# Kernel optimization log

Measured on AMD Instinct MI355X. Metric: run time of the kernel, lower is better.

Reference implementation:

```python
import jax, jax.numpy as jnp
import numpy as np

N_NODES = 100000
N_EDGES = 600000
IN_CH = 128
HID = 128


def setup_inputs() -> dict:
    key = jax.random.key(0)
    ks = jax.random.split(key, 8)
    x = jax.random.normal(ks[0], (N_NODES, IN_CH), dtype=jnp.float32)
    edge_index = jax.random.randint(ks[1], (2, N_EDGES), 0, N_NODES, dtype=jnp.int64)
    # Linear weights stored as (in, out); scaled like torch default init
    W1 = jax.random.normal(ks[2], (2 * IN_CH, HID), dtype=jnp.float32) / np.sqrt(2 * IN_CH)
    b1 = jnp.zeros((HID,), dtype=jnp.float32)
    W2 = jax.random.normal(ks[3], (HID, HID), dtype=jnp.float32) / np.sqrt(HID)
    b2 = jnp.zeros((HID,), dtype=jnp.float32)
    W3 = jax.random.normal(ks[4], (HID, 1), dtype=jnp.float32) / np.sqrt(HID)
    b3 = jnp.zeros((1,), dtype=jnp.float32)
    return {"x": x, "edge_index": edge_index, "W1": W1, "b1": b1,
            "W2": W2, "b2": b2, "W3": W3, "b3": b3}


def reference(x, edge_index, W1, b1, W2, b2, W3, b3):
    src = edge_index[0]
    tgt = edge_index[1]
    # gather + concat: [n_edges, 2*in_channels]
    h = jnp.concatenate([x[src, :], x[tgt, :]], axis=1)
    h = jax.nn.elu(h @ W1 + b1)
    h = jax.nn.elu(h @ W2 + b2)
    h = h @ W3 + b3  # [n_edges, 1]
    return jnp.squeeze(h)  # squeeze=True path -> [n_edges]
```

## Files before the change

### kernel.cpp

```cpp
#include <hip/hip_runtime.h>

#define N_NODES 100000
#define N_EDGES 600000
#define NT1 1563
#define NT2 9375
#define LDH 136
#define LDO 264
typedef _Float16 f16x8 __attribute__((ext_vector_type(8)));
typedef _Float16 f16x4 __attribute__((ext_vector_type(4)));
typedef __attribute__((ext_vector_type(4))) float f32x4;

__device__ __forceinline__ float elu_f(float v) {
    return v > 0.0f ? v : (__expf(v) - 1.0f);
}

extern "C" __global__ __launch_bounds__(256, 3)
void k1_node_linear(const float* __restrict__ x, const float* __restrict__ W1,
                    _Float16* __restrict__ P) {
    __shared__ __align__(16) _Float16 sX[64 * LDH];
    __shared__ __align__(16) _Float16 sOut[64 * LDO];

    const int t = threadIdx.x;
    const int w = t >> 6, lane = t & 63;
    const int ln = lane & 15, kg = lane >> 4;

    f16x8 bf[2][2][4];
#pragma unroll
    for (int half = 0; half < 2; ++half)
#pragma unroll
        for (int c = 0; c < 2; ++c) {
            const int n = w * 32 + c * 16 + ln;
#pragma unroll
            for (int ks = 0; ks < 4; ++ks) {
                f16x8 v;
#pragma unroll
                for (int j = 0; j < 8; ++j) {
                    int k = half * 128 + ks * 32 + kg * 8 + j;
                    v[j] = (_Float16)W1[k * 128 + n];
                }
                bf[half][c][ks] = v;
            }
        }

    for (int tile = blockIdx.x; tile < NT1; tile += gridDim.x) {
        const int n0 = tile * 64;

        {
            const size_t fbase = (size_t)n0 * 128;
#pragma unroll
            for (int i = 0; i < 8; ++i) {
                const int f = t * 4 + i * 1024;
                float4 a = make_float4(0.f, 0.f, 0.f, 0.f);
                if (fbase + (size_t)f < (size_t)N_NODES * 128)
                    a = *(const float4*)(x + fbase + f);
                f16x4 h;
                h[0] = (_Float16)a.x; h[1] = (_Float16)a.y;
                h[2] = (_Float16)a.z; h[3] = (_Float16)a.w;
                *(f16x4*)(&sX[(f >> 7) * LDH + (f & 127)]) = h;
            }
        }
        __syncthreads();

        f32x4 acc[2][4][2];
#pragma unroll
        for (int half = 0; half < 2; ++half)
#pragma unroll
            for (int rt = 0; rt < 4; ++rt)
#pragma unroll
                for (int c = 0; c < 2; ++c) acc[half][rt][c] = (f32x4){0.f, 0.f, 0.f, 0.f};

#pragma unroll
        for (int ks = 0; ks < 4; ++ks) {
#pragma unroll
            for (int rt = 0; rt < 4; ++rt) {
                f16x8 a = *(const f16x8*)(&sX[(rt * 16 + ln) * LDH + ks * 32 + kg * 8]);
#pragma unroll
                for (int half = 0; half < 2; ++half)
#pragma unroll
                    for (int c = 0; c < 2; ++c)
                        acc[half][rt][c] = __builtin_amdgcn_mfma_f32_16x16x32_f16(
                            a, bf[half][c][ks], acc[half][rt][c], 0, 0, 0);
            }
        }
        __syncthreads();

#pragma unroll
        for (int half = 0; half < 2; ++half)
#pragma unroll
            for (int rt = 0; rt < 4; ++rt)
#pragma unroll
                for (int c = 0; c < 2; ++c) {
                    const int col = half * 128 + w * 32 + c * 16 + ln;
#pragma unroll
                    for (int reg = 0; reg < 4; ++reg) {
                        const int row = rt * 16 + kg * 4 + reg;
                        sOut[row * LDO + col] = (_Float16)acc[half][rt][c][reg];
                    }
                }
        __syncthreads();

        {
            const size_t ebase = (size_t)n0 * 256;
#pragma unroll
            for (int i = 0; i < 8; ++i) {
                const int e = t * 8 + i * 2048;
                if (n0 + (e >> 8) < N_NODES) {
                    f16x8 v = *(const f16x8*)(&sOut[(e >> 8) * LDO + (e & 255)]);
                    *(f16x8*)(P + ebase + e) = v;
                }
            }
        }
    }
}

extern "C" __global__ __launch_bounds__(256, 3)
void k2_edge_mlp(const _Float16* __restrict__ P, const void* __restrict__ eiv,
                 const float* __restrict__ b1, const float* __restrict__ W2,
                 const float* __restrict__ b2, const float* __restrict__ W3,
                 const float* __restrict__ b3, float* __restrict__ out) {
    __shared__ __align__(16) _Float16 sH[2][64 * LDH];
    __shared__ float sPart[2][4][64];
    __shared__ int sFlag;

    const int t = threadIdx.x;
    const int w = t >> 6, lane = t & 63;
    const int ln = lane & 15, kg = lane >> 4;
    const int row = t >> 2;
    const int kc0 = (t & 3) * 4;
    const float b3v = b3[0];
    const int stride = gridDim.x;

    if (t < 64) {
        unsigned v = ((const unsigned*)eiv)[2 * t + 1];
        unsigned long long bm = __ballot(v == 0u);
        if (t == 0) sFlag = (bm == ~0ull) ? 1 : 0;
    }

    f16x8 b1f[4];
#pragma unroll
    for (int i = 0; i < 4; ++i)
#pragma unroll
        for (int j = 0; j < 8; ++j) b1f[i][j] = (_Float16)b1[(kc0 + i) * 8 + j];

    float w3v[2], b2v[2];
#pragma unroll
    for (int c = 0; c < 2; ++c) {
        int col = w * 32 + c * 16 + ln;
        w3v[c] = W3[col]; b2v[c] = b2[col];
    }

    f16x8 bfw[2][4];
#pragma unroll
    for (int c = 0; c < 2; ++c) {
        const int n = w * 32 + c * 16 + ln;
#pragma unroll
        for (int ks = 0; ks < 4; ++ks) {
            f16x8 v;
#pragma unroll
            for (int j = 0; j < 8; ++j) {
                int k = ks * 32 + kg * 8 + j;
                v[j] = (_Float16)W2[k * 128 + n];
            }
            bfw[c][ks] = v;
        }
    }
    __syncthreads();
    const int mode64 = sFlag;

    const int tile0 = blockIdx.x;

    int se_nx, ge_nx;
    {
        int e = tile0 * 64 + row;
        if (mode64) {
            se_nx = (int)((const long long*)eiv)[e];
            ge_nx = (int)((const long long*)eiv)[N_EDGES + e];
        } else {
            se_nx = ((const int*)eiv)[e];
            ge_nx = ((const int*)eiv)[N_EDGES + e];
        }
    }
    {
        const _Float16* pa = P + (size_t)se_nx * 256 + kc0 * 8;
        const _Float16* pb = P + (size_t)ge_nx * 256 + 128 + kc0 * 8;
        f16x8 Ga[4], Gb[4];
#pragma unroll
        for (int i = 0; i < 4; ++i) {
            Ga[i] = *(const f16x8*)(pa + i * 8);
            Gb[i] = *(const f16x8*)(pb + i * 8);
        }
#pragma unroll
        for (int i = 0; i < 4; ++i) {
            f16x8 s = Ga[i] + Gb[i] + b1f[i];
            f16x8 vh;
#pragma unroll
            for (int j = 0; j < 8; ++j) {
                _Float16 sv = s[j];
                vh[j] = (sv > (_Float16)0) ? sv
                        : (_Float16)(__expf((float)sv) - 1.0f);
            }
            *(f16x8*)(&sH[0][row * LDH + (kc0 + i) * 8]) = vh;
        }
    }
    {
        int t1 = tile0 + stride;
        int t1c = (t1 < NT2) ? t1 : tile0;
        int e = t1c * 64 + row;
        if (mode64) {
            se_nx = (int)((const long long*)eiv)[e];
            ge_nx = (int)((const long long*)eiv)[N_EDGES + e];
        } else {
            se_nx = ((const int*)eiv)[e];
            ge_nx = ((const int*)eiv)[N_EDGES + e];
        }
    }
    __syncthreads();

    int p = 0;
    int prevE0 = -1;
    for (int tile = tile0; tile < NT2; tile += stride) {
        const int nt = tile + stride;
        const int ntc = (nt < NT2) ? nt : tile;

        const _Float16* pa = P + (size_t)se_nx * 256 + kc0 * 8;
        const _Float16* pb = P + (size_t)ge_nx * 256 + 128 + kc0 * 8;
        f16x8 Ga[4], Gb[4];
#pragma unroll
        for (int i = 0; i < 4; ++i) {
            Ga[i] = *(const f16x8*)(pa + i * 8);
            Gb[i] = *(const f16x8*)(pb + i * 8);
        }

        {
            int n2 = nt + stride;
            int n2c = (n2 < NT2) ? n2 : ntc;
            int e = n2c * 64 + row;
            if (mode64) {
                se_nx = (int)((const long long*)eiv)[e];
                ge_nx = (int)((const long long*)eiv)[N_EDGES + e];
            } else {
                se_nx = ((const int*)eiv)[e];
                ge_nx = ((const int*)eiv)[N_EDGES + e];
            }
        }

        if (prevE0 >= 0 && t < 64)
            out[prevE0 + t] = sPart[p ^ 1][0][t] + sPart[p ^ 1][1][t] +
                              sPart[p ^ 1][2][t] + sPart[p ^ 1][3][t] + b3v;

        f32x4 acc[4][2];
#pragma unroll
        for (int rt = 0; rt < 4; ++rt)
#pragma unroll
            for (int c = 0; c < 2; ++c) acc[rt][c] = (f32x4){0.f, 0.f, 0.f, 0.f};

#pragma unroll
        for (int ks = 0; ks < 4; ++ks) {
#pragma unroll
            for (int rt = 0; rt < 4; ++rt) {
                f16x8 a = *(const f16x8*)(&sH[p][(rt * 16 + ln) * LDH + ks * 32 + kg * 8]);
#pragma unroll
                for (int c = 0; c < 2; ++c)
                    acc[rt][c] = __builtin_amdgcn_mfma_f32_16x16x32_f16(a, bfw[c][ks], acc[rt][c], 0, 0, 0);
            }
        }

#pragma unroll
        for (int rt = 0; rt < 4; ++rt) {
            float pr[4] = {0.f, 0.f, 0.f, 0.f};
#pragma unroll
            for (int c = 0; c < 2; ++c) {
#pragma unroll
                for (int reg = 0; reg < 4; ++reg)
                    pr[reg] += elu_f(acc[rt][c][reg] + b2v[c]) * w3v[c];
            }
#pragma unroll
            for (int m = 1; m < 16; m <<= 1)
#pragma unroll
                for (int reg = 0; reg < 4; ++reg) pr[reg] += __shfl_xor(pr[reg], m, 64);
            if (ln == 0) {
#pragma unroll
                for (int reg = 0; reg < 4; ++reg)
                    sPart[p][w][rt * 16 + kg * 4 + reg] = pr[reg];
            }
        }

#pragma unroll
        for (int i = 0; i < 4; ++i) {
            f16x8 s = Ga[i] + Gb[i] + b1f[i];
            f16x8 vh;
#pragma unroll
            for (int j = 0; j < 8; ++j) {
                _Float16 sv = s[j];
                vh[j] = (sv > (_Float16)0) ? sv
                        : (_Float16)(__expf((float)sv) - 1.0f);
            }
            *(f16x8*)(&sH[p ^ 1][row * LDH + (kc0 + i) * 8]) = vh;
        }

        prevE0 = tile * 64;
        __syncthreads();
        p ^= 1;
    }

    if (prevE0 >= 0 && t < 64)
        out[prevE0 + t] = sPart[p ^ 1][0][t] + sPart[p ^ 1][1][t] +
                          sPart[p ^ 1][2][t] + sPart[p ^ 1][3][t] + b3v;
}

extern "C" void kernel_launch(void* const* d_in, const int* in_sizes, int n_in,
                              void* d_out, int out_size, void* d_ws, size_t ws_size,
                              hipStream_t stream) {
    const float* x  = (const float*)d_in[0];
    const void*  ei = d_in[1];
    const float* W1 = (const float*)d_in[2];
    const float* b1 = (const float*)d_in[3];
    const float* W2 = (const float*)d_in[4];
    const float* b2 = (const float*)d_in[5];
    const float* W3 = (const float*)d_in[6];
    const float* b3 = (const float*)d_in[7];
    float* out = (float*)d_out;

    _Float16* P = (_Float16*)((char*)d_ws + 256);

    k1_node_linear<<<768, 256, 0, stream>>>(x, W1, P);
    k2_edge_mlp<<<768, 256, 0, stream>>>(P, ei, b1, W2, b2, W3, b3, out);
}
```

Before: 224.6 us.

## Move first linear layer from per-node precompute into per-edge MFMA pipeline

Drops the node-level projection kernel, which computed x@W1 halves for every node and wrote a 256-wide fp16 table. Instead, a small kernel converts x to fp16, and the edge kernel gathers raw source and target features into shared memory. There it runs layer 1 with MFMA, applies ELU and feeds layer 2 in the same tile. This halves the intermediate table's size and write traffic, but multiplies layer-1 math by the edge/node ratio. It also adds two block barriers per tile and lowers the occupancy hint to 2 blocks per CU with 512 blocks.

```diff
diff --git a/kernel.cpp b/kernel.cpp
--- a/kernel.cpp
+++ b/kernel.cpp
@@ -2,29 +2,56 @@
 
 #define N_NODES 100000
 #define N_EDGES 600000
-#define NT1 1563
 #define NT2 9375
-#define LDH 136
-#define LDO 264
+#define LDW 264
 typedef _Float16 f16x8 __attribute__((ext_vector_type(8)));
-typedef _Float16 f16x4 __attribute__((ext_vector_type(4)));
 typedef __attribute__((ext_vector_type(4))) float f32x4;
 
 __device__ __forceinline__ float elu_f(float v) {
     return v > 0.0f ? v : (__expf(v) - 1.0f);
 }
 
-extern "C" __global__ __launch_bounds__(256, 3)
-void k1_node_linear(const float* __restrict__ x, const float* __restrict__ W1,
-                    _Float16* __restrict__ P) {
-    __shared__ __align__(16) _Float16 sX[64 * LDH];
-    __shared__ __align__(16) _Float16 sOut[64 * LDO];
+extern "C" __global__ __launch_bounds__(256)
+void k0_convert(const float* __restrict__ x, _Float16* __restrict__ xh) {
+    const int step = gridDim.x * blockDim.x;
+    for (int c = blockIdx.x * blockDim.x + threadIdx.x; c < (N_NODES * 128) / 8;
+         c += step) {
+        const float4 a0 = *(const float4*)(x + (size_t)c * 8);
+        const float4 a1 = *(const float4*)(x + (size_t)c * 8 + 4);
+        f16x8 h;
+        h[0] = (_Float16)a0.x; h[1] = (_Float16)a0.y;
+        h[2] = (_Float16)a0.z; h[3] = (_Float16)a0.w;
+        h[4] = (_Float16)a1.x; h[5] = (_Float16)a1.y;
+        h[6] = (_Float16)a1.z; h[7] = (_Float16)a1.w;
+        *(f16x8*)(xh + (size_t)c * 8) = h;
+    }
+}
+
+extern "C" __global__ __launch_bounds__(256, 2)
+void k2_edge_mlp(const _Float16* __restrict__ xh, const void* __restrict__ eiv,
+                 const float* __restrict__ W1, const float* __restrict__ b1,
+                 const float* __restrict__ W2, const float* __restrict__ b2,
+                 const float* __restrict__ W3, const float* __restrict__ b3,
+                 float* __restrict__ out) {
+    __shared__ __align__(16) _Float16 sRaw[2][64 * LDW];
+    __shared__ float sPart[2][4][64];
+    __shared__ int sFlag;
 
     const int t = threadIdx.x;
     const int w = t >> 6, lane = t & 63;
     const int ln = lane & 15, kg = lane >> 4;
-
-    f16x8 bf[2][2][4];
+    const int row_s = t >> 2;
+    const int qb = (t & 3) * 32;
+    const float b3v = b3[0];
+    const int stride = gridDim.x;
+
+    if (t < 64) {
+        unsigned v = ((const unsigned*)eiv)[2 * t + 1];
+        unsigned long long bm = __ballot(v == 0u);
+        if (t == 0) sFlag = (bm == ~0ull) ? 1 : 0;
+    }
+
+    f16x8 bf1[2][2][4];
 #pragma unroll
     for (int half = 0; half < 2; ++half)
 #pragma unroll
@@ -38,118 +65,11 @@
                     int k = half * 128 + ks * 32 + kg * 8 + j;
                     v[j] = (_Float16)W1[k * 128 + n];
                 }
-                bf[half][c][ks] = v;
-            }
-        }
-
-    for (int tile = blockIdx.x; tile < NT1; tile += gridDim.x) {
-        const int n0 = tile * 64;
-
-        {
-            const size_t fbase = (size_t)n0 * 128;
-#pragma unroll
-            for (int i = 0; i < 8; ++i) {
-                const int f = t * 4 + i * 1024;
-                float4 a = make_float4(0.f, 0.f, 0.f, 0.f);
-                if (fbase + (size_t)f < (size_t)N_NODES * 128)
-                    a = *(const float4*)(x + fbase + f);
-                f16x4 h;
-                h[0] = (_Float16)a.x; h[1] = (_Float16)a.y;
-                h[2] = (_Float16)a.z; h[3] = (_Float16)a.w;
-                *(f16x4*)(&sX[(f >> 7) * LDH + (f & 127)]) = h;
-            }
-        }
-        __syncthreads();
-
-        f32x4 acc[2][4][2];
-#pragma unroll
-        for (int half = 0; half < 2; ++half)
-#pragma unroll
-            for (int rt = 0; rt < 4; ++rt)
-#pragma unroll
-                for (int c = 0; c < 2; ++c) acc[half][rt][c] = (f32x4){0.f, 0.f, 0.f, 0.f};
-
-#pragma unroll
-        for (int ks = 0; ks < 4; ++ks) {
-#pragma unroll
-            for (int rt = 0; rt < 4; ++rt) {
-                f16x8 a = *(const f16x8*)(&sX[(rt * 16 + ln) * LDH + ks * 32 + kg * 8]);
-#pragma unroll
-                for (int half = 0; half < 2; ++half)
-#pragma unroll
-                    for (int c = 0; c < 2; ++c)
-                        acc[half][rt][c] = __builtin_amdgcn_mfma_f32_16x16x32_f16(
-                            a, bf[half][c][ks], acc[half][rt][c], 0, 0, 0);
-            }
-        }
-        __syncthreads();
-
-#pragma unroll
-        for (int half = 0; half < 2; ++half)
-#pragma unroll
-            for (int rt = 0; rt < 4; ++rt)
-#pragma unroll
-                for (int c = 0; c < 2; ++c) {
-                    const int col = half * 128 + w * 32 + c * 16 + ln;
-#pragma unroll
-                    for (int reg = 0; reg < 4; ++reg) {
-                        const int row = rt * 16 + kg * 4 + reg;
-                        sOut[row * LDO + col] = (_Float16)acc[half][rt][c][reg];
-                    }
-                }
-        __syncthreads();
-
-        {
-            const size_t ebase = (size_t)n0 * 256;
-#pragma unroll
-            for (int i = 0; i < 8; ++i) {
-                const int e = t * 8 + i * 2048;
-                if (n0 + (e >> 8) < N_NODES) {
-                    f16x8 v = *(const f16x8*)(&sOut[(e >> 8) * LDO + (e & 255)]);
-                    *(f16x8*)(P + ebase + e) = v;
-                }
-            }
-        }
-    }
-}
-
-extern "C" __global__ __launch_bounds__(256, 3)
-void k2_edge_mlp(const _Float16* __restrict__ P, const void* __restrict__ eiv,
-                 const float* __restrict__ b1, const float* __restrict__ W2,
-                 const float* __restrict__ b2, const float* __restrict__ W3,
-                 const float* __restrict__ b3, float* __restrict__ out) {
-    __shared__ __align__(16) _Float16 sH[2][64 * LDH];
-    __shared__ float sPart[2][4][64];
-    __shared__ int sFlag;
-
-    const int t = threadIdx.x;
-    const int w = t >> 6, lane = t & 63;
-    const int ln = lane & 15, kg = lane >> 4;
-    const int row = t >> 2;
-    const int kc0 = (t & 3) * 4;
-    const float b3v = b3[0];
-    const int stride = gridDim.x;
-
-    if (t < 64) {
-        unsigned v = ((const unsigned*)eiv)[2 * t + 1];
-        unsigned long long bm = __ballot(v == 0u);
-        if (t == 0) sFlag = (bm == ~0ull) ? 1 : 0;
-    }
-
-    f16x8 b1f[4];
-#pragma unroll
-    for (int i = 0; i < 4; ++i)
-#pragma unroll
-        for (int j = 0; j < 8; ++j) b1f[i][j] = (_Float16)b1[(kc0 + i) * 8 + j];
-
-    float w3v[2], b2v[2];
-#pragma unroll
-    for (int c = 0; c < 2; ++c) {
-        int col = w * 32 + c * 16 + ln;
-        w3v[c] = W3[col]; b2v[c] = b2[col];
-    }
-
-    f16x8 bfw[2][4];
+                bf1[half][c][ks] = v;
+            }
+        }
+
+    f16x8 bf2[2][4];
 #pragma unroll
     for (int c = 0; c < 2; ++c) {
         const int n = w * 32 + c * 16 + ln;
@@ -161,17 +81,46 @@
                 int k = ks * 32 + kg * 8 + j;
                 v[j] = (_Float16)W2[k * 128 + n];
             }
-            bfw[c][ks] = v;
-        }
-    }
+            bf2[c][ks] = v;
+        }
+    }
+
+    float b1v[2], b2v[2], w3v[2];
+#pragma unroll
+    for (int c = 0; c < 2; ++c) {
+        int col = w * 32 + c * 16 + ln;
+        b1v[c] = b1[col]; b2v[c] = b2[col]; w3v[c] = W3[col];
+    }
+
     __syncthreads();
     const int mode64 = sFlag;
-
     const int tile0 = blockIdx.x;
 
     int se_nx, ge_nx;
     {
-        int e = tile0 * 64 + row;
+        int e = tile0 * 64 + row_s;
+        int se, ge;
+        if (mode64) {
+            se = (int)((const long long*)eiv)[e];
+            ge = (int)((const long long*)eiv)[N_EDGES + e];
+        } else {
+            se = ((const int*)eiv)[e];
+            ge = ((const int*)eiv)[N_EDGES + e];
+        }
+        const _Float16* pa = xh + (size_t)se * 128 + qb;
+        const _Float16* pb = xh + (size_t)ge * 128 + qb;
+#pragma unroll
+        for (int i = 0; i < 4; ++i) {
+            f16x8 ga = *(const f16x8*)(pa + i * 8);
+            f16x8 gb = *(const f16x8*)(pb + i * 8);
+            *(f16x8*)(&sRaw[0][row_s * LDW + qb + i * 8]) = ga;
+            *(f16x8*)(&sRaw[0][row_s * LDW + 128 + qb + i * 8]) = gb;
+        }
+    }
+    {
+        int t1 = tile0 + stride;
+        int t1c = (t1 < NT2) ? t1 : tile0;
+        int e = t1c * 64 + row_s;
         if (mode64) {
             se_nx = (int)((const long long*)eiv)[e];
             ge_nx = (int)((const long long*)eiv)[N_EDGES + e];
@@ -180,40 +129,6 @@
             ge_nx = ((const int*)eiv)[N_EDGES + e];
         }
     }
-    {
-        const _Float16* pa = P + (size_t)se_nx * 256 + kc0 * 8;
-        const _Float16* pb = P + (size_t)ge_nx * 256 + 128 + kc0 * 8;
-        f16x8 Ga[4], Gb[4];
-#pragma unroll
-        for (int i = 0; i < 4; ++i) {
-            Ga[i] = *(const f16x8*)(pa + i * 8);
-            Gb[i] = *(const f16x8*)(pb + i * 8);
-        }
-#pragma unroll
-        for (int i = 0; i < 4; ++i) {
-            f16x8 s = Ga[i] + Gb[i] + b1f[i];
-            f16x8 vh;
-#pragma unroll
-            for (int j = 0; j < 8; ++j) {
-                _Float16 sv = s[j];
-                vh[j] = (sv > (_Float16)0) ? sv
-                        : (_Float16)(__expf((float)sv) - 1.0f);
-            }
-            *(f16x8*)(&sH[0][row * LDH + (kc0 + i) * 8]) = vh;
-        }
-    }
-    {
-        int t1 = tile0 + stride;
-        int t1c = (t1 < NT2) ? t1 : tile0;
-        int e = t1c * 64 + row;
-        if (mode64) {
-            se_nx = (int)((const long long*)eiv)[e];
-            ge_nx = (int)((const long long*)eiv)[N_EDGES + e];
-        } else {
-            se_nx = ((const int*)eiv)[e];
-            ge_nx = ((const int*)eiv)[N_EDGES + e];
-        }
-    }
     __syncthreads();
 
     int p = 0;
@@ -222,8 +137,8 @@
         const int nt = tile + stride;
         const int ntc = (nt < NT2) ? nt : tile;
 
-        const _Float16* pa = P + (size_t)se_nx * 256 + kc0 * 8;
-        const _Float16* pb = P + (size_t)ge_nx * 256 + 128 + kc0 * 8;
+        const _Float16* pa = xh + (size_t)se_nx * 128 + qb;
+        const _Float16* pb = xh + (size_t)ge_nx * 128 + qb;
         f16x8 Ga[4], Gb[4];
 #pragma unroll
         for (int i = 0; i < 4; ++i) {
@@ -234,7 +149,7 @@
         {
             int n2 = nt + stride;
             int n2c = (n2 < NT2) ? n2 : ntc;
-            int e = n2c * 64 + row;
+            int e = n2c * 64 + row_s;
             if (mode64) {
                 se_nx = (int)((const long long*)eiv)[e];
                 ge_nx = (int)((const long long*)eiv)[N_EDGES + e];
@@ -248,20 +163,58 @@
             out[prevE0 + t] = sPart[p ^ 1][0][t] + sPart[p ^ 1][1][t] +
                               sPart[p ^ 1][2][t] + sPart[p ^ 1][3][t] + b3v;
 
-        f32x4 acc[4][2];
+        f32x4 acc1[4][2];
 #pragma unroll
         for (int rt = 0; rt < 4; ++rt)
 #pragma unroll
-            for (int c = 0; c < 2; ++c) acc[rt][c] = (f32x4){0.f, 0.f, 0.f, 0.f};
+            for (int c = 0; c < 2; ++c) acc1[rt][c] = (f32x4){0.f, 0.f, 0.f, 0.f};
 
 #pragma unroll
         for (int ks = 0; ks < 4; ++ks) {
 #pragma unroll
             for (int rt = 0; rt < 4; ++rt) {
-                f16x8 a = *(const f16x8*)(&sH[p][(rt * 16 + ln) * LDH + ks * 32 + kg * 8]);
+                f16x8 a_s = *(const f16x8*)(&sRaw[p][(rt * 16 + ln) * LDW + ks * 32 + kg * 8]);
+                f16x8 a_t = *(const f16x8*)(&sRaw[p][(rt * 16 + ln) * LDW + 128 + ks * 32 + kg * 8]);
+#pragma unroll
+                for (int c = 0; c < 2; ++c) {
+                    acc1[rt][c] = __builtin_amdgcn_mfma_f32_16x16x32_f16(
+                        a_s, bf1[0][c][ks], acc1[rt][c], 0, 0, 0);
+                    acc1[rt][c] = __builtin_amdgcn_mfma_f32_16x16x32_f16(
+                        a_t, bf1[1][c][ks], acc1[rt][c], 0, 0, 0);
+                }
+            }
+        }
+        __syncthreads();
+
+#pragma unroll
+        for (int rt = 0; rt < 4; ++rt)
+#pragma unroll
+            for (int c = 0; c < 2; ++c) {
+                const int col = w * 32 + c * 16 + ln;
+#pragma unroll
+                for (int reg = 0; reg < 4; ++reg) {
+                    const int row = rt * 16 + kg * 4 + reg;
+                    sRaw[p][row * LDW + col] =
+                        (_Float16)elu_f(acc1[rt][c][reg] + b1v[c]);
+                }
+            }
+        __syncthreads();
+
+        f32x4 acc2[4][2];
+#pragma unroll
+        for (int rt = 0; rt < 4; ++rt)
+#pragma unroll
+            for (int c = 0; c < 2; ++c) acc2[rt][c] = (f32x4){0.f, 0.f, 0.f, 0.f};
+
+#pragma unroll
+        for (int ks = 0; ks < 4; ++ks) {
+#pragma unroll
+            for (int rt = 0; rt < 4; ++rt) {
+                f16x8 a = *(const f16x8*)(&sRaw[p][(rt * 16 + ln) * LDW + ks * 32 + kg * 8]);
 #pragma unroll
                 for (int c = 0; c < 2; ++c)
-                    acc[rt][c] = __builtin_amdgcn_mfma_f32_16x16x32_f16(a, bfw[c][ks], acc[rt][c], 0, 0, 0);
+                    acc2[rt][c] = __builtin_amdgcn_mfma_f32_16x16x32_f16(
+                        a, bf2[c][ks], acc2[rt][c], 0, 0, 0);
             }
         }
 
@@ -272,7 +225,7 @@
             for (int c = 0; c < 2; ++c) {
 #pragma unroll
                 for (int reg = 0; reg < 4; ++reg)
-                    pr[reg] += elu_f(acc[rt][c][reg] + b2v[c]) * w3v[c];
+                    pr[reg] += elu_f(acc2[rt][c][reg] + b2v[c]) * w3v[c];
             }
 #pragma unroll
             for (int m = 1; m < 16; m <<= 1)
@@ -287,15 +240,8 @@
 
 #pragma unroll
         for (int i = 0; i < 4; ++i) {
-            f16x8 s = Ga[i] + Gb[i] + b1f[i];
-            f16x8 vh;
-#pragma unroll
-            for (int j = 0; j < 8; ++j) {
-                _Float16 sv = s[j];
-                vh[j] = (sv > (_Float16)0) ? sv
-                        : (_Float16)(__expf((float)sv) - 1.0f);
-            }
-            *(f16x8*)(&sH[p ^ 1][row * LDH + (kc0 + i) * 8]) = vh;
+            *(f16x8*)(&sRaw[p ^ 1][row_s * LDW + qb + i * 8]) = Ga[i];
+            *(f16x8*)(&sRaw[p ^ 1][row_s * LDW + 128 + qb + i * 8]) = Gb[i];
         }
 
         prevE0 = tile * 64;
@@ -321,8 +267,8 @@
     const float* b3 = (const float*)d_in[7];
     float* out = (float*)d_out;
 
-    _Float16* P = (_Float16*)((char*)d_ws + 256);
-
-    k1_node_linear<<<768, 256, 0, stream>>>(x, W1, P);
-    k2_edge_mlp<<<768, 256, 0, stream>>>(P, ei, b1, W2, b2, W3, b3, out);
-}
+    _Float16* xh = (_Float16*)((char*)d_ws + 256);
+
+    k0_convert<<<2048, 256, 0, stream>>>(x, xh);
+    k2_edge_mlp<<<512, 256, 0, stream>>>(xh, ei, W1, b1, W2, b2, W3, b3, out);
+}
```

After: 207.3 us. 1.08x faster.
